# Kernel tuning notes

Measured on AMD Instinct MI355X. Metric: run time of the kernel, lower is better.

The kernel has to match this reference:

```python
import jax, jax.numpy as jnp
import numpy as np

HALF = 512   # dim // 2 == hyper_dim // 2
DIM = 1024
EPS = 1e-6


def _forward(hl, hr, xw, xh,
             qU_w, qU_b, qWu_w, qWu_b, qWb_w, qWb_b,
             kU_w, kU_b, kWu_w, kWu_b, kWb_w, kWb_b,
             alpha, beta,
             hU_w, hU_b, hWu_w, hWu_b, hWb_w, hWb_b,
             lU_w, lU_b, lWu_w, lWu_b, lWb_w, lWb_b):
    # x: (B, dim)
    x = jnp.concatenate([hl, hr], axis=1)
    # hlr: (B, 2, dim//2), xh1: (B, 1, hyper_dim//2)
    hlr = jnp.stack([hl, hr], axis=1)
    xh1 = xh[:, None, :]
    # HyperLinear: U(x) * Wu(xh) + Wb(xh); weights stored (in, out)
    q = (hlr @ qU_w + qU_b) * (xh1 @ qWu_w + qWu_b) + (xh1 @ qWb_w + qWb_b)
    k = (hlr @ kU_w + kU_b) * (xh1 @ kWu_w + kWu_b) + (xh1 @ kWb_w + kWb_b)
    # tiny 2x2 attention per sample
    scores = jax.nn.softmax(
        jnp.einsum('bqd,bkd->bqk', q, k) / jnp.sqrt(jnp.float32(HALF)), axis=-1)
    x = x + jnp.einsum('bqk,bkd->bqd', scores, hlr).reshape(x.shape[0], -1)
    # Norm: torch .std() is unbiased (ddof=1)
    mean = jnp.mean(x, axis=-1, keepdims=True)
    std = jnp.std(x, axis=-1, keepdims=True, ddof=1)
    x = alpha * (x - mean) / (std + EPS) + beta
    # hidden(x, xh) + leaf(xw, xh), both HyperLinear -> (B, dim//2)
    hidden = (x @ hU_w + hU_b) * (xh @ hWu_w + hWu_b) + (xh @ hWb_w + hWb_b)
    leaf = (xw @ lU_w + lU_b) * (xh @ lWu_w + lWu_b) + (xh @ lWb_w + lWb_b)
    return hidden + leaf


def setup_inputs() -> dict:
    key = jax.random.key(0)
    ks = jax.random.split(key, 32)
    B = 32768
    f32 = jnp.float32

    def w(k, shape, s=0.05):
        return jax.random.normal(k, shape, dtype=f32) * s

    inp = {
        'hl': jax.random.normal(ks[0], (B, HALF), dtype=f32),
        'hr': jax.random.normal(ks[1], (B, HALF), dtype=f32),
        'xw': jax.random.normal(ks[2], (B, DIM), dtype=f32),
        'xh': jax.random.normal(ks[3], (B, HALF), dtype=f32),
        # q_linear: HyperLinear(512, 512) with hyper
        'qU_w': w(ks[4], (HALF, HALF)), 'qU_b': w(ks[5], (HALF,)),
        'qWu_w': w(ks[6], (HALF, HALF)), 'qWu_b': w(ks[7], (HALF,)),
        'qWb_w': w(ks[8], (HALF, HALF)), 'qWb_b': w(ks[9], (HALF,)),
        # k_linear
        'kU_w': w(ks[10], (HALF, HALF)), 'kU_b': w(ks[11], (HALF,)),
        'kWu_w': w(ks[12], (HALF, HALF)), 'kWu_b': w(ks[13], (HALF,)),
        'kWb_w': w(ks[14], (HALF, HALF)), 'kWb_b': w(ks[15], (HALF,)),
        # Norm params over dim
        'alpha': jnp.ones((DIM,), dtype=f32),
        'beta': jnp.zeros((DIM,), dtype=f32),
        # hidden: HyperLinear(512, 1024 -> 512)
        'hU_w': w(ks[16], (DIM, HALF)), 'hU_b': w(ks[17], (HALF,)),
        'hWu_w': w(ks[18], (HALF, HALF)), 'hWu_b': w(ks[19], (HALF,)),
        'hWb_w': w(ks[20], (HALF, HALF)), 'hWb_b': w(ks[21], (HALF,)),
        # leaf: HyperLinear(512, 1024 -> 512)
        'lU_w': w(ks[22], (DIM, HALF)), 'lU_b': w(ks[23], (HALF,)),
        'lWu_w': w(ks[24], (HALF, HALF)), 'lWu_b': w(ks[25], (HALF,)),
        'lWb_w': w(ks[26], (HALF, HALF)), 'lWb_b': w(ks[27], (HALF,)),
    }
    return inp


def reference(hl, hr, xw, xh,
              qU_w, qU_b, qWu_w, qWu_b, qWb_w, qWb_b,
              kU_w, kU_b, kWu_w, kWu_b, kWb_w, kWb_b,
              alpha, beta,
              hU_w, hU_b, hWu_w, hWu_b, hWb_w, hWb_b,
              lU_w, lU_b, lWu_w, lWu_b, lWb_w, lWb_b):
    return _forward(hl, hr, xw, xh,
                    qU_w, qU_b, qWu_w, qWu_b, qWb_w, qWb_b,
                    kU_w, kU_b, kWu_w, kWu_b, kWb_w, kWb_b,
                    alpha, beta,
                    hU_w, hU_b, hWu_w, hWu_b, hWb_w, hWb_b,
                    lU_w, lU_b, lWu_w, lWu_b, lWb_w, lWb_b)
```

## Files before the change

kernel.cpp:

```cpp
#include <hip/hip_runtime.h>


typedef __attribute__((ext_vector_type(4))) float floatx4;
typedef __attribute__((ext_vector_type(8))) short shortx8;

#define NROWS 32768
#define MT 32
#define NT 64
#define BK 32
#define APAD 40
#define WMAT 262144

__device__ __forceinline__ unsigned short f2bf(float f){
  union { float f; unsigned u; } v; v.f = f;
  return (unsigned short)((v.u + 0x7fffu + ((v.u >> 16) & 1u)) >> 16);
}

struct TrArgs {
  const float* src[14];
  int off[14];
  int sc[14];
};

__global__ __launch_bounds__(256) void ktr(TrArgs ta, const float* __restrict__ alpha,
                                           unsigned short* __restrict__ wt){
  __shared__ float tile[32][33];
  const int t  = blockIdx.x >> 8;
  const int ti = blockIdx.x & 255;
  const int n0 = (ti & 15) * 32, k0 = (ti >> 4) * 32;
  const float* src = ta.src[t];
  const int off = ta.off[t], sc = ta.sc[t];
  const int r = threadIdx.x >> 5, c = threadIdx.x & 31;
#pragma unroll
  for (int p = 0; p < 4; p++){
    const int kr = p*8 + r;
    float v = src[(size_t)(off + k0 + kr)*512 + n0 + c];
    if (sc) v *= alpha[off + k0 + kr];
    tile[kr][c] = v;
  }
  __syncthreads();
#pragma unroll
  for (int p = 0; p < 4; p++){
    const int nr = p*8 + r;
    wt[(size_t)t*WMAT + (size_t)(n0+nr)*512 + k0 + c] = f2bf(tile[c][nr]);
  }
}

__global__ __launch_bounds__(256) void kst(const float* __restrict__ alpha, const float* __restrict__ beta,
                                           const float* __restrict__ hU,
                                           float* __restrict__ sp, float* __restrict__ tp){
  const int n = blockIdx.x*256 + threadIdx.x;
  float s = 0.f, t = 0.f;
  for (int k = 0; k < 1024; k++){
    const float wv = hU[(size_t)k*512 + n];
    s += alpha[k]*wv; t += beta[k]*wv;
  }
  sp[n] = s; tp[n] = t;
}

__global__ __launch_bounds__(256) void kstats(const float* __restrict__ hl, const float* __restrict__ hr,
                                              float* __restrict__ stats){
  const int w = threadIdx.x >> 6, lane = threadIdx.x & 63;
  const int row = blockIdx.x*4 + w;
  const float4* A  = (const float4*)(hl + (size_t)row*512);
  const float4* Bv = (const float4*)(hr + (size_t)row*512);
  float s1=0,s2=0,q1=0,q2=0,xc=0;
#pragma unroll
  for (int j=0;j<2;j++){
    const float4 a = A[lane + 64*j];
    const float4 b = Bv[lane + 64*j];
    s1 += a.x+a.y+a.z+a.w;
    s2 += b.x+b.y+b.z+b.w;
    q1 += a.x*a.x + a.y*a.y + a.z*a.z + a.w*a.w;
    q2 += b.x*b.x + b.y*b.y + b.z*b.z + b.w*b.w;
    xc += a.x*b.x + a.y*b.y + a.z*b.z + a.w*b.w;
  }
  for (int off=32; off; off>>=1){
    s1 += __shfl_down(s1,off); s2 += __shfl_down(s2,off);
    q1 += __shfl_down(q1,off); q2 += __shfl_down(q2,off);
    xc += __shfl_down(xc,off);
  }
  if (lane == 0){
    float* st = stats + (size_t)row*8;
    st[0]=s1; st[1]=s2; st[2]=q1; st[3]=q2; st[4]=xc;
  }
}

struct K1LDS {
  union alignas(16) {
    unsigned short stage[3*1280 + 6*2560];
    float proj[8*2112];
  } u;
  float sred[32*8*4];
};

__global__ __launch_bounds__(256,2) void k1(
    const float* __restrict__ hl, const float* __restrict__ hr, const float* __restrict__ xh,
    const unsigned short* __restrict__ wt,
    const float* __restrict__ qUb, const float* __restrict__ qWub, const float* __restrict__ qWbb,
    const float* __restrict__ kUb, const float* __restrict__ kWub, const float* __restrict__ kWbb,
    const float* __restrict__ stats, float* __restrict__ scal)
{
  __shared__ K1LDS sm;
  const int tid = threadIdx.x, w = tid >> 6, lane = tid & 63;
  const int row0 = blockIdx.x * MT;
  unsigned short* stA = sm.u.stage;
  unsigned short* stB = sm.u.stage + 3*1280;
  floatx4 acc[4][4];
  floatx4 zf; zf[0]=0.f; zf[1]=0.f; zf[2]=0.f; zf[3]=0.f;
  float s0=0.f, s1=0.f, s2=0.f, s3=0.f;
  const int erow = tid >> 3, esub = tid & 7;

  for (int dt = 0; dt < 8; dt++){
    const int d0 = dt * NT;
#pragma unroll
    for (int i=0;i<4;i++)
#pragma unroll
      for (int ns=0;ns<4;ns++) acc[i][ns] = zf;

    for (int cch = 0; cch < 16; cch++){
      const int k0 = cch * BK;
#pragma unroll
      for (int q0 = 0; q0 < 3; q0++){
        const int q = q0*256 + tid;
        const int a = q >> 8, rem = q & 255, r = rem >> 3, c4 = rem & 7;
        const float* src = (a==0) ? hl : ((a==1) ? hr : xh);
        const float4 v = *(const float4*)(src + (size_t)(row0 + r)*512 + k0 + c4*4);
        unsigned long long pk = (unsigned long long)f2bf(v.x)
                              | ((unsigned long long)f2bf(v.y) << 16)
                              | ((unsigned long long)f2bf(v.z) << 32)
                              | ((unsigned long long)f2bf(v.w) << 48);
        *(unsigned long long*)(stA + a*1280 + r*APAD + c4*4) = pk;
      }
#pragma unroll
      for (int q0 = 0; q0 < 6; q0++){
        const int q = q0*256 + tid;
        const int m = q >> 8, rem = q & 255, r = rem >> 2, c8 = rem & 3;
        *(uint4*)(stB + m*2560 + r*APAD + c8*8) =
            *(const uint4*)(wt + (size_t)m*WMAT + (size_t)(d0 + r)*512 + k0 + c8*8);
      }
      __syncthreads();
      shortx8 bfr[4];
#pragma unroll
      for (int i=0;i<4;i++){
        const int p = (w*4 + i) >> 1, ms = i & 1;
        if ((i & 1) == 0){
          const int bidx = (p < 4) ? (p >> 1) : (p - 2);
#pragma unroll
          for (int ns=0;ns<4;ns++)
            bfr[ns] = *(const shortx8*)(stB + bidx*2560 + (ns*16 + (lane & 15))*APAD + (lane >> 4)*8);
        }
        const int aidx = (p < 4) ? (p & 1) : 2;
        const shortx8 af = *(const shortx8*)(stA + aidx*1280 + (ms*16 + (lane & 15))*APAD + (lane >> 4)*8);
#pragma unroll
        for (int ns=0;ns<4;ns++)
          acc[i][ns] = __builtin_amdgcn_mfma_f32_16x16x32_bf16(af, bfr[ns], acc[i][ns], 0, 0, 0);
      }
      __syncthreads();
    }
#pragma unroll
    for (int i=0;i<4;i++){
      const int p = (w*4 + i) >> 1, ms = i & 1;
#pragma unroll
      for (int ns=0;ns<4;ns++)
#pragma unroll
        for (int r=0;r<4;r++)
          sm.u.proj[p*2112 + (ms*16 + (lane >> 4)*4 + r)*66 + ns*16 + (lane & 15)] = acc[i][ns][r];
    }
    __syncthreads();
#pragma unroll
    for (int j=0;j<8;j++){
      const int dd = esub*8 + j, gd = d0 + dd;
      const float ul = sm.u.proj[0*2112 + erow*66 + dd];
      const float ur = sm.u.proj[1*2112 + erow*66 + dd];
      const float vl = sm.u.proj[2*2112 + erow*66 + dd];
      const float vr = sm.u.proj[3*2112 + erow*66 + dd];
      const float pm = sm.u.proj[4*2112 + erow*66 + dd];
      const float pn = sm.u.proj[5*2112 + erow*66 + dd];
      const float pm2= sm.u.proj[6*2112 + erow*66 + dd];
      const float pn2= sm.u.proj[7*2112 + erow*66 + dd];
      const float f1 = pm + qWub[gd], f2 = pn + qWbb[gd];
      const float g1 = pm2 + kWub[gd], g2 = pn2 + kWbb[gd];
      const float ub = qUb[gd], kb = kUb[gd];
      const float ql = (ul + ub)*f1 + f2;
      const float qr = (ur + ub)*f1 + f2;
      const float kl = (vl + kb)*g1 + g2;
      const float kr = (vr + kb)*g1 + g2;
      s0 += ql*kl; s1 += ql*kr; s2 += qr*kl; s3 += qr*kr;
    }
    __syncthreads();
  }
  {
    float* sr = sm.sred + (erow*8 + esub)*4;
    sr[0]=s0; sr[1]=s1; sr[2]=s2; sr[3]=s3;
  }
  __syncthreads();
  if (tid < MT){
    const int row = tid;
    float t00=0,t01=0,t10=0,t11=0;
#pragma unroll
    for (int j=0;j<8;j++){
      const float* p = sm.sred + (row*8 + j)*4;
      t00+=p[0]; t01+=p[1]; t10+=p[2]; t11+=p[3];
    }
    const float isq = 0.044194173824159216f;
    t00*=isq; t01*=isq; t10*=isq; t11*=isq;
    const float m0 = fmaxf(t00,t01), m1 = fmaxf(t10,t11);
    const float e00 = expf(t00-m0), e01 = expf(t01-m0);
    const float e10 = expf(t10-m1), e11 = expf(t11-m1);
    const float p00 = e00/(e00+e01), p01 = e01/(e00+e01);
    const float p10 = e10/(e10+e11), p11 = e11/(e10+e11);
    const float* st = stats + (size_t)(row0+row)*8;
    const float S1=st[0], S2=st[1], Q1=st[2], Q2=st[3], Xc=st[4];
    const float a0=1.f+p00, a1=p01, b0=p10, b1=1.f+p11;
    const float mean = ((a0+b0)*S1 + (a1+b1)*S2) * (1.f/1024.f);
    const float ssq = (a0*a0+b0*b0)*Q1 + (a1*a1+b1*b1)*Q2 + 2.f*(a0*a1+b0*b1)*Xc;
    const float var = (ssq - 1024.f*mean*mean) * (1.f/1023.f);
    const float inv = 1.f/(sqrtf(fmaxf(var,0.f)) + 1e-6f);
    float* so = scal + (size_t)(row0+row)*8;
    so[0]=p00; so[1]=p01; so[2]=p10; so[3]=p11; so[4]=mean; so[5]=inv;
  }
}

struct K2LDS {
  union alignas(16) {
    unsigned short stage[5*1280 + 8*2560];
    float proj[9*2112];
  } u;
};

__global__ __launch_bounds__(256,2) void k2(
    const float* __restrict__ hl, const float* __restrict__ hr,
    const float* __restrict__ xh, const float* __restrict__ xw,
    const unsigned short* __restrict__ wt,
    const float* __restrict__ sp, const float* __restrict__ tp,
    const float* __restrict__ hUb, const float* __restrict__ hWub, const float* __restrict__ hWbb,
    const float* __restrict__ lUb, const float* __restrict__ lWub, const float* __restrict__ lWbb,
    const float* __restrict__ scal, float* __restrict__ out)
{
  __shared__ K2LDS sm;
  const int tid = threadIdx.x, w = tid >> 6, lane = tid & 63;
  const int row0 = blockIdx.x * MT;
  unsigned short* stA = sm.u.stage;
  unsigned short* stB = sm.u.stage + 5*1280;
  const int erow = tid >> 3, ej0 = (tid & 7)*8;
  const float* sl = scal + (size_t)(row0 + erow)*8;
  const float p00 = sl[0], p01 = sl[1], p10 = sl[2], p11 = sl[3], mean = sl[4], inv = sl[5];
  const float a0 = 1.f + p00, a1 = p01, b0 = p10, b1 = 1.f + p11;
  floatx4 acc[5][4];
  floatx4 zf; zf[0]=0.f; zf[1]=0.f; zf[2]=0.f; zf[3]=0.f;

  for (int dt = 0; dt < 8; dt++){
    const int d0 = dt * NT;
#pragma unroll
    for (int i=0;i<5;i++)
#pragma unroll
      for (int ns=0;ns<4;ns++) acc[i][ns] = zf;

    for (int cch = 0; cch < 16; cch++){
      const int k0 = cch * BK;
#pragma unroll
      for (int q0 = 0; q0 < 5; q0++){
        const int q = q0*256 + tid;
        const int a = q >> 8, rem = q & 255, r = rem >> 3, c4 = rem & 7;
        const float* srcb = (a==0) ? hl : ((a==1) ? hr : ((a==2) ? xh : xw));
        const int stride = (a >= 3) ? 1024 : 512;
        const int coff = (a == 4) ? 512 : 0;
        const float4 v = *(const float4*)(srcb + (size_t)(row0 + r)*stride + coff + k0 + c4*4);
        unsigned long long pk = (unsigned long long)f2bf(v.x)
                              | ((unsigned long long)f2bf(v.y) << 16)
                              | ((unsigned long long)f2bf(v.z) << 32)
                              | ((unsigned long long)f2bf(v.w) << 48);
        *(unsigned long long*)(stA + a*1280 + r*APAD + c4*4) = pk;
      }
#pragma unroll
      for (int q0 = 0; q0 < 8; q0++){
        const int q = q0*256 + tid;
        const int m = q >> 8, rem = q & 255, r = rem >> 2, c8 = rem & 3;
        *(uint4*)(stB + m*2560 + r*APAD + c8*8) =
            *(const uint4*)(wt + (size_t)(m+6)*WMAT + (size_t)(d0 + r)*512 + k0 + c8*8);
      }
      __syncthreads();
      shortx8 bfr[4];
      int prevB = -1;
#pragma unroll
      for (int i=0;i<5;i++){
        const int wtask = w*5 + i, p = wtask >> 1, ms = wtask & 1;
        const int bl = (p<4) ? (p>>1) : ((p<6) ? (p-2) : ((p<8) ? p : (p-4)));
        if (bl != prevB){
#pragma unroll
          for (int ns=0;ns<4;ns++)
            bfr[ns] = *(const shortx8*)(stB + bl*2560 + (ns*16 + (lane&15))*APAD + (lane>>4)*8);
          prevB = bl;
        }
        const int am = (p<4) ? (p&1) : ((p<8) ? 2 : (p-5));
        const shortx8 af = *(const shortx8*)(stA + am*1280 + (ms*16 + (lane&15))*APAD + (lane>>4)*8);
#pragma unroll
        for (int ns=0;ns<4;ns++)
          acc[i][ns] = __builtin_amdgcn_mfma_f32_16x16x32_bf16(af, bfr[ns], acc[i][ns], 0, 0, 0);
      }
      __syncthreads();
    }
#pragma unroll
    for (int i=0;i<5;i++){
      const int wtask = w*5 + i, p = wtask >> 1, ms = wtask & 1;
      const int slot = (p == 9) ? 8 : p;
#pragma unroll
      for (int ns=0;ns<4;ns++)
#pragma unroll
        for (int r=0;r<4;r++){
          float* dst = &sm.u.proj[slot*2112 + (ms*16 + (lane>>4)*4 + r)*66 + ns*16 + (lane & 15)];
          if (p == 9) *dst += acc[i][ns][r]; else *dst = acc[i][ns][r];
        }
    }
    __syncthreads();
    float res[8];
#pragma unroll
    for (int j=0;j<8;j++){
      const int dd = ej0 + j, gd = d0 + dd;
      const float A1 = sm.u.proj[0*2112 + erow*66 + dd];
      const float A2 = sm.u.proj[1*2112 + erow*66 + dd];
      const float A3 = sm.u.proj[2*2112 + erow*66 + dd];
      const float A4 = sm.u.proj[3*2112 + erow*66 + dd];
      const float Hm = sm.u.proj[4*2112 + erow*66 + dd];
      const float Hb = sm.u.proj[5*2112 + erow*66 + dd];
      const float Lm = sm.u.proj[6*2112 + erow*66 + dd];
      const float Lb = sm.u.proj[7*2112 + erow*66 + dd];
      const float Lu = sm.u.proj[8*2112 + erow*66 + dd];
      const float attnU = a0*A1 + a1*A2 + b0*A3 + b1*A4;
      const float xlnU = inv*(attnU - mean*sp[gd]) + tp[gd] + hUb[gd];
      const float hid = xlnU*(Hm + hWub[gd]) + (Hb + hWbb[gd]);
      const float lf = (Lu + lUb[gd])*(Lm + lWub[gd]) + (Lb + lWbb[gd]);
      res[j] = hid + lf;
    }
    float4 r0; r0.x=res[0]; r0.y=res[1]; r0.z=res[2]; r0.w=res[3];
    float4 r1; r1.x=res[4]; r1.y=res[5]; r1.z=res[6]; r1.w=res[7];
    float4* op = (float4*)(out + (size_t)(row0+erow)*512 + d0 + ej0);
    op[0] = r0; op[1] = r1;
    __syncthreads();
  }
}

extern "C" void kernel_launch(void* const* d_in, const int* in_sizes, int n_in,
                              void* d_out, int out_size, void* d_ws, size_t ws_size,
                              hipStream_t stream)
{
  const float* hl    = (const float*)d_in[0];
  const float* hr    = (const float*)d_in[1];
  const float* xw    = (const float*)d_in[2];
  const float* xh    = (const float*)d_in[3];
  const float* qU_w  = (const float*)d_in[4];
  const float* qU_b  = (const float*)d_in[5];
  const float* qWu_w = (const float*)d_in[6];
  const float* qWu_b = (const float*)d_in[7];
  const float* qWb_w = (const float*)d_in[8];
  const float* qWb_b = (const float*)d_in[9];
  const float* kU_w  = (const float*)d_in[10];
  const float* kU_b  = (const float*)d_in[11];
  const float* kWu_w = (const float*)d_in[12];
  const float* kWu_b = (const float*)d_in[13];
  const float* kWb_w = (const float*)d_in[14];
  const float* kWb_b = (const float*)d_in[15];
  const float* alpha = (const float*)d_in[16];
  const float* beta  = (const float*)d_in[17];
  const float* hU_w  = (const float*)d_in[18];
  const float* hU_b  = (const float*)d_in[19];
  const float* hWu_w = (const float*)d_in[20];
  const float* hWu_b = (const float*)d_in[21];
  const float* hWb_w = (const float*)d_in[22];
  const float* hWb_b = (const float*)d_in[23];
  const float* lU_w  = (const float*)d_in[24];
  const float* lU_b  = (const float*)d_in[25];
  const float* lWu_w = (const float*)d_in[26];
  const float* lWu_b = (const float*)d_in[27];
  const float* lWb_w = (const float*)d_in[28];
  const float* lWb_b = (const float*)d_in[29];

  char* ws = (char*)d_ws;
  unsigned short* wt = (unsigned short*)ws;
  float* sp    = (float*)(ws + 7340032);
  float* tp    = sp + 512;
  float* stats = (float*)(ws + 7344128);
  float* scal  = (float*)(ws + 8392704);

  TrArgs ta;
  const float* wsrc[14] = {qU_w,kU_w,qWu_w,qWb_w,kWu_w,kWb_w,hU_w,hU_w,hWu_w,hWb_w,lU_w,lU_w,lWu_w,lWb_w};
  const int woff[14] = {0,0,0,0,0,0,0,512,0,0,0,512,0,0};
  const int wsc[14]  = {0,0,0,0,0,0,1,1,0,0,0,0,0,0};
  for (int i=0;i<14;i++){ ta.src[i]=wsrc[i]; ta.off[i]=woff[i]; ta.sc[i]=wsc[i]; }

  ktr   <<<dim3(14*256),  dim3(256), 0, stream>>>(ta, alpha, wt);
  kst   <<<dim3(2),       dim3(256), 0, stream>>>(alpha, beta, hU_w, sp, tp);
  kstats<<<dim3(NROWS/4), dim3(256), 0, stream>>>(hl, hr, stats);
  k1    <<<dim3(NROWS/MT),dim3(256), 0, stream>>>(hl, hr, xh, wt,
            qU_b, qWu_b, qWb_b, kU_b, kWu_b, kWb_b, stats, scal);
  k2    <<<dim3(NROWS/MT),dim3(256), 0, stream>>>(hl, hr, xh, xw, wt, sp, tp,
            hU_b, hWu_b, hWb_b, lU_b, lWu_b, lWb_b, scal, (float*)d_out);
}
```

Measured before the change: 1.312 ms.

## Pre-convert activations to bf16, use direct global-to-LDS loads, keep epilogue in registers

Adds kernels that convert hl/hr/xh/xw to bf16 once in workspace, with the hl/hr conversion fused into the stats kernel. The GEMM kernels then stage A and B tiles with global_load_lds instead of per-tile fp32 loads and conversion. k1 is retiled to 128-wide output tiles and its epilogue computes q·k partial sums from accumulator registers with shuffle reductions rather than spilling projections to LDS. k2 likewise computes its output directly from registers. This removes the LDS round trip and the repeated conversions, at the cost of extra workspace traffic and a fallback path when the workspace is too small.

```diff
diff --git a/kernel.cpp b/kernel.cpp
--- a/kernel.cpp
+++ b/kernel.cpp
@@ -5,15 +5,24 @@
 typedef __attribute__((ext_vector_type(8))) short shortx8;
 
 #define NROWS 32768
-#define MT 32
-#define NT 64
-#define BK 32
-#define APAD 40
 #define WMAT 262144
+
+#define MFMA16(a,b,c) __builtin_amdgcn_mfma_f32_16x16x32_bf16(a,b,c,0,0,0)
 
 __device__ __forceinline__ unsigned short f2bf(float f){
   union { float f; unsigned u; } v; v.f = f;
   return (unsigned short)((v.u + 0x7fffu + ((v.u >> 16) & 1u)) >> 16);
+}
+
+__device__ __forceinline__ unsigned long long pack4(float4 v){
+  return (unsigned long long)f2bf(v.x) | ((unsigned long long)f2bf(v.y)<<16)
+       | ((unsigned long long)f2bf(v.z)<<32) | ((unsigned long long)f2bf(v.w)<<48);
+}
+
+__device__ __forceinline__ void gl_lds16(const void* g, void* l){
+  __builtin_amdgcn_global_load_lds(
+      (const __attribute__((address_space(1))) unsigned int*)g,
+      (__attribute__((address_space(3))) unsigned int*)l, 16, 0, 0);
 }
 
 struct TrArgs {
@@ -69,8 +78,7 @@
   for (int j=0;j<2;j++){
     const float4 a = A[lane + 64*j];
     const float4 b = Bv[lane + 64*j];
-    s1 += a.x+a.y+a.z+a.w;
-    s2 += b.x+b.y+b.z+b.w;
+    s1 += a.x+a.y+a.z+a.w;  s2 += b.x+b.y+b.z+b.w;
     q1 += a.x*a.x + a.y*a.y + a.z*a.z + a.w*a.w;
     q2 += b.x*b.x + b.y*b.y + b.z*b.z + b.w*b.w;
     xc += a.x*b.x + a.y*b.y + a.z*b.z + a.w*b.w;
@@ -86,122 +94,190 @@
   }
 }
 
-struct K1LDS {
-  union alignas(16) {
-    unsigned short stage[3*1280 + 6*2560];
-    float proj[8*2112];
-  } u;
-  float sred[32*8*4];
-};
-
+__global__ __launch_bounds__(256) void kconv_stats(const float* __restrict__ hl, const float* __restrict__ hr,
+                                                   unsigned short* __restrict__ hlb, unsigned short* __restrict__ hrb,
+                                                   float* __restrict__ stats){
+  const int w = threadIdx.x >> 6, lane = threadIdx.x & 63;
+  const int row = blockIdx.x*4 + w;
+  const float4* A  = (const float4*)(hl + (size_t)row*512);
+  const float4* Bv = (const float4*)(hr + (size_t)row*512);
+  float s1=0,s2=0,q1=0,q2=0,xc=0;
+#pragma unroll
+  for (int j=0;j<2;j++){
+    const float4 a = A[lane + 64*j];
+    const float4 b = Bv[lane + 64*j];
+    s1 += a.x+a.y+a.z+a.w;  s2 += b.x+b.y+b.z+b.w;
+    q1 += a.x*a.x + a.y*a.y + a.z*a.z + a.w*a.w;
+    q2 += b.x*b.x + b.y*b.y + b.z*b.z + b.w*b.w;
+    xc += a.x*b.x + a.y*b.y + a.z*b.z + a.w*b.w;
+    *(unsigned long long*)(hlb + (size_t)row*512 + (lane + 64*j)*4) = pack4(a);
+    *(unsigned long long*)(hrb + (size_t)row*512 + (lane + 64*j)*4) = pack4(b);
+  }
+  for (int off=32; off; off>>=1){
+    s1 += __shfl_down(s1,off); s2 += __shfl_down(s2,off);
+    q1 += __shfl_down(q1,off); q2 += __shfl_down(q2,off);
+    xc += __shfl_down(xc,off);
+  }
+  if (lane == 0){
+    float* st = stats + (size_t)row*8;
+    st[0]=s1; st[1]=s2; st[2]=q1; st[3]=q2; st[4]=xc;
+  }
+}
+
+__global__ __launch_bounds__(256) void kact(const float* __restrict__ xh, const float* __restrict__ xw,
+                                            unsigned short* __restrict__ xhb, unsigned short* __restrict__ xwb){
+  const int bid = blockIdx.x;
+  const float* src; unsigned short* dst; size_t base;
+  if (bid < 8192){ src = xh; dst = xhb; base = (size_t)bid*2048; }
+  else           { src = xw; dst = xwb; base = (size_t)(bid-8192)*2048; }
+  const size_t i = base + (size_t)threadIdx.x*8;
+  const float4 v0 = *(const float4*)(src + i);
+  const float4 v1 = *(const float4*)(src + i + 4);
+  unsigned long long p0 = pack4(v0), p1 = pack4(v1);
+  *(unsigned long long*)(dst + i)     = p0;
+  *(unsigned long long*)(dst + i + 4) = p1;
+}
+
+template<int PRE>
 __global__ __launch_bounds__(256,2) void k1(
     const float* __restrict__ hl, const float* __restrict__ hr, const float* __restrict__ xh,
+    const unsigned short* __restrict__ hlb, const unsigned short* __restrict__ hrb,
+    const unsigned short* __restrict__ xhb,
     const unsigned short* __restrict__ wt,
     const float* __restrict__ qUb, const float* __restrict__ qWub, const float* __restrict__ qWbb,
     const float* __restrict__ kUb, const float* __restrict__ kWub, const float* __restrict__ kWbb,
     const float* __restrict__ stats, float* __restrict__ scal)
 {
-  __shared__ K1LDS sm;
+  __shared__ __align__(16) unsigned short Ash[3*1024];
+  __shared__ __align__(16) unsigned short Bsh[6*4096];
+  __shared__ float sred[512];
   const int tid = threadIdx.x, w = tid >> 6, lane = tid & 63;
-  const int row0 = blockIdx.x * MT;
-  unsigned short* stA = sm.u.stage;
-  unsigned short* stB = sm.u.stage + 3*1280;
-  floatx4 acc[4][4];
+  const int cq = lane & 15, cr = lane >> 4;
+  const int row0 = blockIdx.x * 32;
+
+  for (int i = tid; i < 512; i += 256) sred[i] = 0.f;
+
+  floatx4 acc[8][2][2];
   floatx4 zf; zf[0]=0.f; zf[1]=0.f; zf[2]=0.f; zf[3]=0.f;
-  float s0=0.f, s1=0.f, s2=0.f, s3=0.f;
-  const int erow = tid >> 3, esub = tid & 7;
-
-  for (int dt = 0; dt < 8; dt++){
-    const int d0 = dt * NT;
-#pragma unroll
-    for (int i=0;i<4;i++)
-#pragma unroll
-      for (int ns=0;ns<4;ns++) acc[i][ns] = zf;
-
-    for (int cch = 0; cch < 16; cch++){
-      const int k0 = cch * BK;
-#pragma unroll
-      for (int q0 = 0; q0 < 3; q0++){
-        const int q = q0*256 + tid;
-        const int a = q >> 8, rem = q & 255, r = rem >> 3, c4 = rem & 7;
-        const float* src = (a==0) ? hl : ((a==1) ? hr : xh);
-        const float4 v = *(const float4*)(src + (size_t)(row0 + r)*512 + k0 + c4*4);
-        unsigned long long pk = (unsigned long long)f2bf(v.x)
-                              | ((unsigned long long)f2bf(v.y) << 16)
-                              | ((unsigned long long)f2bf(v.z) << 32)
-                              | ((unsigned long long)f2bf(v.w) << 48);
-        *(unsigned long long*)(stA + a*1280 + r*APAD + c4*4) = pk;
-      }
-#pragma unroll
-      for (int q0 = 0; q0 < 6; q0++){
-        const int q = q0*256 + tid;
-        const int m = q >> 8, rem = q & 255, r = rem >> 2, c8 = rem & 3;
-        *(uint4*)(stB + m*2560 + r*APAD + c8*8) =
-            *(const uint4*)(wt + (size_t)m*WMAT + (size_t)(d0 + r)*512 + k0 + c8*8);
+
+#pragma unroll 1
+  for (int dt = 0; dt < 4; dt++){
+    const int d0 = dt * 128;
+#pragma unroll
+    for (int p=0;p<8;p++)
+#pragma unroll
+      for (int ms=0;ms<2;ms++){ acc[p][ms][0]=zf; acc[p][ms][1]=zf; }
+
+#pragma unroll 1
+    for (int cc = 0; cc < 16; cc++){
+      const int k0 = cc * 32;
+      if (PRE){
+#pragma unroll
+        for (int j=0;j<2;j++){
+          const int idx = j*256 + tid;
+          if (idx < 384){
+            const int a = idx>>7, wi = idx&127, r = wi>>2, kg = wi&3;
+            const unsigned short* s = (a==0) ? hlb : ((a==1) ? hrb : xhb);
+            gl_lds16(s + (size_t)(row0+r)*512 + k0 + kg*8, Ash + idx*8);
+          }
+        }
+      } else {
+#pragma unroll
+        for (int a=0;a<3;a++){
+          const int r = tid>>3, c4 = tid&7;
+          const float* s = (a==0) ? hl : ((a==1) ? hr : xh);
+          const float4 v = *(const float4*)(s + (size_t)(row0+r)*512 + k0 + c4*4);
+          *(unsigned long long*)(Ash + a*1024 + r*32 + c4*4) = pack4(v);
+        }
+      }
+#pragma unroll
+      for (int j=0;j<12;j++){
+        const int idx = j*256 + tid;
+        const int m = idx>>9, wi = idx&511, r = wi>>2, kg = wi&3;
+        gl_lds16(wt + (size_t)m*WMAT + (size_t)(d0+r)*512 + k0 + kg*8, Bsh + idx*8);
       }
       __syncthreads();
-      shortx8 bfr[4];
-#pragma unroll
-      for (int i=0;i<4;i++){
-        const int p = (w*4 + i) >> 1, ms = i & 1;
-        if ((i & 1) == 0){
-          const int bidx = (p < 4) ? (p >> 1) : (p - 2);
-#pragma unroll
-          for (int ns=0;ns<4;ns++)
-            bfr[ns] = *(const shortx8*)(stB + bidx*2560 + (ns*16 + (lane & 15))*APAD + (lane >> 4)*8);
-        }
-        const int aidx = (p < 4) ? (p & 1) : 2;
-        const shortx8 af = *(const shortx8*)(stA + aidx*1280 + (ms*16 + (lane & 15))*APAD + (lane >> 4)*8);
-#pragma unroll
-        for (int ns=0;ns<4;ns++)
-          acc[i][ns] = __builtin_amdgcn_mfma_f32_16x16x32_bf16(af, bfr[ns], acc[i][ns], 0, 0, 0);
+      shortx8 af[3][2], bf[6];
+#pragma unroll
+      for (int a=0;a<3;a++)
+#pragma unroll
+        for (int ms=0;ms<2;ms++)
+          af[a][ms] = *(const shortx8*)(Ash + a*1024 + (ms*16+cq)*32 + cr*8);
+#pragma unroll
+      for (int n=0;n<2;n++){
+#pragma unroll
+        for (int m=0;m<6;m++)
+          bf[m] = *(const shortx8*)(Bsh + m*4096 + (w*32 + n*16 + cq)*32 + cr*8);
+#pragma unroll
+        for (int ms=0;ms<2;ms++){
+          acc[0][ms][n] = MFMA16(af[0][ms], bf[0], acc[0][ms][n]);
+          acc[1][ms][n] = MFMA16(af[1][ms], bf[0], acc[1][ms][n]);
+          acc[2][ms][n] = MFMA16(af[0][ms], bf[1], acc[2][ms][n]);
+          acc[3][ms][n] = MFMA16(af[1][ms], bf[1], acc[3][ms][n]);
+          acc[4][ms][n] = MFMA16(af[2][ms], bf[2], acc[4][ms][n]);
+          acc[5][ms][n] = MFMA16(af[2][ms], bf[3], acc[5][ms][n]);
+          acc[6][ms][n] = MFMA16(af[2][ms], bf[4], acc[6][ms][n]);
+          acc[7][ms][n] = MFMA16(af[2][ms], bf[5], acc[7][ms][n]);
+        }
       }
       __syncthreads();
     }
-#pragma unroll
-    for (int i=0;i<4;i++){
-      const int p = (w*4 + i) >> 1, ms = i & 1;
-#pragma unroll
-      for (int ns=0;ns<4;ns++)
+    float qub[2], qwu[2], qwb[2], kub[2], kwu[2], kwb[2];
+#pragma unroll
+    for (int n=0;n<2;n++){
+      const int col = d0 + w*32 + n*16 + cq;
+      qub[n]=qUb[col]; qwu[n]=qWub[col]; qwb[n]=qWbb[col];
+      kub[n]=kUb[col]; kwu[n]=kWub[col]; kwb[n]=kWbb[col];
+    }
+    float sc[2][4][4];
+#pragma unroll
+    for (int ms=0;ms<2;ms++)
+#pragma unroll
+      for (int r=0;r<4;r++){ sc[ms][r][0]=0.f; sc[ms][r][1]=0.f; sc[ms][r][2]=0.f; sc[ms][r][3]=0.f; }
+#pragma unroll
+    for (int ms=0;ms<2;ms++)
+#pragma unroll
+      for (int n=0;n<2;n++)
+#pragma unroll
+        for (int r=0;r<4;r++){
+          const float ul = acc[0][ms][n][r], ur = acc[1][ms][n][r];
+          const float vl = acc[2][ms][n][r], vr = acc[3][ms][n][r];
+          const float f1 = acc[4][ms][n][r] + qwu[n], f2 = acc[5][ms][n][r] + qwb[n];
+          const float g1 = acc[6][ms][n][r] + kwu[n], g2 = acc[7][ms][n][r] + kwb[n];
+          const float ql = (ul + qub[n])*f1 + f2, qr = (ur + qub[n])*f1 + f2;
+          const float kl = (vl + kub[n])*g1 + g2, kr = (vr + kub[n])*g1 + g2;
+          sc[ms][r][0] += ql*kl; sc[ms][r][1] += ql*kr;
+          sc[ms][r][2] += qr*kl; sc[ms][r][3] += qr*kr;
+        }
+#pragma unroll
+    for (int b=1;b<16;b<<=1)
+#pragma unroll
+      for (int ms=0;ms<2;ms++)
 #pragma unroll
         for (int r=0;r<4;r++)
-          sm.u.proj[p*2112 + (ms*16 + (lane >> 4)*4 + r)*66 + ns*16 + (lane & 15)] = acc[i][ns][r];
+#pragma unroll
+          for (int c=0;c<4;c++)
+            sc[ms][r][c] += __shfl_xor(sc[ms][r][c], b);
+    if (cq == 0){
+#pragma unroll
+      for (int ms=0;ms<2;ms++)
+#pragma unroll
+        for (int r=0;r<4;r++){
+          const int row = ms*16 + cr*4 + r;
+#pragma unroll
+          for (int c=0;c<4;c++)
+            sred[w*128 + row*4 + c] += sc[ms][r][c];
+        }
     }
-    __syncthreads();
-#pragma unroll
-    for (int j=0;j<8;j++){
-      const int dd = esub*8 + j, gd = d0 + dd;
-      const float ul = sm.u.proj[0*2112 + erow*66 + dd];
-      const float ur = sm.u.proj[1*2112 + erow*66 + dd];
-      const float vl = sm.u.proj[2*2112 + erow*66 + dd];
-      const float vr = sm.u.proj[3*2112 + erow*66 + dd];
-      const float pm = sm.u.proj[4*2112 + erow*66 + dd];
-      const float pn = sm.u.proj[5*2112 + erow*66 + dd];
-      const float pm2= sm.u.proj[6*2112 + erow*66 + dd];
-      const float pn2= sm.u.proj[7*2112 + erow*66 + dd];
-      const float f1 = pm + qWub[gd], f2 = pn + qWbb[gd];
-      const float g1 = pm2 + kWub[gd], g2 = pn2 + kWbb[gd];
-      const float ub = qUb[gd], kb = kUb[gd];
-      const float ql = (ul + ub)*f1 + f2;
-      const float qr = (ur + ub)*f1 + f2;
-      const float kl = (vl + kb)*g1 + g2;
-      const float kr = (vr + kb)*g1 + g2;
-      s0 += ql*kl; s1 += ql*kr; s2 += qr*kl; s3 += qr*kr;
-    }
-    __syncthreads();
-  }
-  {
-    float* sr = sm.sred + (erow*8 + esub)*4;
-    sr[0]=s0; sr[1]=s1; sr[2]=s2; sr[3]=s3;
   }
   __syncthreads();
-  if (tid < MT){
+  if (tid < 32){
     const int row = tid;
     float t00=0,t01=0,t10=0,t11=0;
 #pragma unroll
-    for (int j=0;j<8;j++){
-      const float* p = sm.sred + (row*8 + j)*4;
-      t00+=p[0]; t01+=p[1]; t10+=p[2]; t11+=p[3];
+    for (int w2=0;w2<4;w2++){
+      const int base = w2*128 + row*4;
+      t00+=sred[base+0]; t01+=sred[base+1]; t10+=sred[base+2]; t11+=sred[base+3];
     }
     const float isq = 0.044194173824159216f;
     t00*=isq; t01*=isq; t10*=isq; t11*=isq;
@@ -222,122 +298,117 @@
   }
 }
 
-struct K2LDS {
-  union alignas(16) {
-    unsigned short stage[5*1280 + 8*2560];
-    float proj[9*2112];
-  } u;
-};
-
+template<int PRE>
 __global__ __launch_bounds__(256,2) void k2(
     const float* __restrict__ hl, const float* __restrict__ hr,
     const float* __restrict__ xh, const float* __restrict__ xw,
+    const unsigned short* __restrict__ hlb, const unsigned short* __restrict__ hrb,
+    const unsigned short* __restrict__ xhb, const unsigned short* __restrict__ xwb,
     const unsigned short* __restrict__ wt,
     const float* __restrict__ sp, const float* __restrict__ tp,
     const float* __restrict__ hUb, const float* __restrict__ hWub, const float* __restrict__ hWbb,
     const float* __restrict__ lUb, const float* __restrict__ lWub, const float* __restrict__ lWbb,
     const float* __restrict__ scal, float* __restrict__ out)
 {
-  __shared__ K2LDS sm;
+  __shared__ __align__(16) unsigned short Ash[5*1024];
+  __shared__ __align__(16) unsigned short Bsh[8*2048];
+  __shared__ float scs[256];
   const int tid = threadIdx.x, w = tid >> 6, lane = tid & 63;
-  const int row0 = blockIdx.x * MT;
-  unsigned short* stA = sm.u.stage;
-  unsigned short* stB = sm.u.stage + 5*1280;
-  const int erow = tid >> 3, ej0 = (tid & 7)*8;
-  const float* sl = scal + (size_t)(row0 + erow)*8;
-  const float p00 = sl[0], p01 = sl[1], p10 = sl[2], p11 = sl[3], mean = sl[4], inv = sl[5];
-  const float a0 = 1.f + p00, a1 = p01, b0 = p10, b1 = 1.f + p11;
-  floatx4 acc[5][4];
+  const int cq = lane & 15, cr = lane >> 4;
+  const int row0 = blockIdx.x * 32;
+
+  scs[tid] = scal[(size_t)row0*8 + tid];
+
+  floatx4 acc[10][2];
   floatx4 zf; zf[0]=0.f; zf[1]=0.f; zf[2]=0.f; zf[3]=0.f;
 
+#pragma unroll 1
   for (int dt = 0; dt < 8; dt++){
-    const int d0 = dt * NT;
-#pragma unroll
-    for (int i=0;i<5;i++)
-#pragma unroll
-      for (int ns=0;ns<4;ns++) acc[i][ns] = zf;
-
-    for (int cch = 0; cch < 16; cch++){
-      const int k0 = cch * BK;
-#pragma unroll
-      for (int q0 = 0; q0 < 5; q0++){
-        const int q = q0*256 + tid;
-        const int a = q >> 8, rem = q & 255, r = rem >> 3, c4 = rem & 7;
-        const float* srcb = (a==0) ? hl : ((a==1) ? hr : ((a==2) ? xh : xw));
-        const int stride = (a >= 3) ? 1024 : 512;
-        const int coff = (a == 4) ? 512 : 0;
-        const float4 v = *(const float4*)(srcb + (size_t)(row0 + r)*stride + coff + k0 + c4*4);
-        unsigned long long pk = (unsigned long long)f2bf(v.x)
-                              | ((unsigned long long)f2bf(v.y) << 16)
-                              | ((unsigned long long)f2bf(v.z) << 32)
-                              | ((unsigned long long)f2bf(v.w) << 48);
-        *(unsigned long long*)(stA + a*1280 + r*APAD + c4*4) = pk;
-      }
-#pragma unroll
-      for (int q0 = 0; q0 < 8; q0++){
-        const int q = q0*256 + tid;
-        const int m = q >> 8, rem = q & 255, r = rem >> 2, c8 = rem & 3;
-        *(uint4*)(stB + m*2560 + r*APAD + c8*8) =
-            *(const uint4*)(wt + (size_t)(m+6)*WMAT + (size_t)(d0 + r)*512 + k0 + c8*8);
+    const int d0 = dt * 64;
+#pragma unroll
+    for (int p=0;p<10;p++){ acc[p][0]=zf; acc[p][1]=zf; }
+
+#pragma unroll 1
+    for (int cc = 0; cc < 16; cc++){
+      const int k0 = cc * 32;
+      if (PRE){
+#pragma unroll
+        for (int j=0;j<3;j++){
+          const int idx = j*256 + tid;
+          if (idx < 640){
+            const int a = idx>>7, wi = idx&127, r = wi>>2, kg = wi&3;
+            const unsigned short* s;
+            size_t off;
+            if (a < 3){ s = (a==0) ? hlb : ((a==1) ? hrb : xhb);
+                        off = (size_t)(row0+r)*512 + k0 + kg*8; }
+            else      { s = xwb;
+                        off = (size_t)(row0+r)*1024 + (a==4 ? 512 : 0) + k0 + kg*8; }
+            gl_lds16(s + off, Ash + idx*8);
+          }
+        }
+      } else {
+#pragma unroll
+        for (int a=0;a<5;a++){
+          const int r = tid>>3, c4 = tid&7;
+          const float* s = (a==0) ? hl : ((a==1) ? hr : ((a==2) ? xh : xw));
+          const int stride = (a>=3) ? 1024 : 512;
+          const int coff = (a==4) ? 512 : 0;
+          const float4 v = *(const float4*)(s + (size_t)(row0+r)*stride + coff + k0 + c4*4);
+          *(unsigned long long*)(Ash + a*1024 + r*32 + c4*4) = pack4(v);
+        }
+      }
+#pragma unroll
+      for (int j=0;j<8;j++){
+        const int idx = j*256 + tid;
+        const int m = idx>>8, wi = idx&255, r = wi>>2, kg = wi&3;
+        gl_lds16(wt + (size_t)(6+m)*WMAT + (size_t)(d0+r)*512 + k0 + kg*8, Bsh + idx*8);
       }
       __syncthreads();
-      shortx8 bfr[4];
-      int prevB = -1;
-#pragma unroll
-      for (int i=0;i<5;i++){
-        const int wtask = w*5 + i, p = wtask >> 1, ms = wtask & 1;
-        const int bl = (p<4) ? (p>>1) : ((p<6) ? (p-2) : ((p<8) ? p : (p-4)));
-        if (bl != prevB){
-#pragma unroll
-          for (int ns=0;ns<4;ns++)
-            bfr[ns] = *(const shortx8*)(stB + bl*2560 + (ns*16 + (lane&15))*APAD + (lane>>4)*8);
-          prevB = bl;
-        }
-        const int am = (p<4) ? (p&1) : ((p<8) ? 2 : (p-5));
-        const shortx8 af = *(const shortx8*)(stA + am*1280 + (ms*16 + (lane&15))*APAD + (lane>>4)*8);
-#pragma unroll
-        for (int ns=0;ns<4;ns++)
-          acc[i][ns] = __builtin_amdgcn_mfma_f32_16x16x32_bf16(af, bfr[ns], acc[i][ns], 0, 0, 0);
+      shortx8 af[5][2], bf[8];
+#pragma unroll
+      for (int a=0;a<5;a++)
+#pragma unroll
+        for (int ms=0;ms<2;ms++)
+          af[a][ms] = *(const shortx8*)(Ash + a*1024 + (ms*16+cq)*32 + cr*8);
+#pragma unroll
+      for (int m=0;m<8;m++)
+        bf[m] = *(const shortx8*)(Bsh + m*2048 + (w*16 + cq)*32 + cr*8);
+#pragma unroll
+      for (int ms=0;ms<2;ms++){
+        acc[0][ms] = MFMA16(af[0][ms], bf[0], acc[0][ms]);
+        acc[1][ms] = MFMA16(af[1][ms], bf[0], acc[1][ms]);
+        acc[2][ms] = MFMA16(af[0][ms], bf[1], acc[2][ms]);
+        acc[3][ms] = MFMA16(af[1][ms], bf[1], acc[3][ms]);
+        acc[4][ms] = MFMA16(af[2][ms], bf[2], acc[4][ms]);
+        acc[5][ms] = MFMA16(af[2][ms], bf[3], acc[5][ms]);
+        acc[6][ms] = MFMA16(af[2][ms], bf[6], acc[6][ms]);
+        acc[7][ms] = MFMA16(af[2][ms], bf[7], acc[7][ms]);
+        acc[8][ms] = MFMA16(af[3][ms], bf[4], acc[8][ms]);
+        acc[9][ms] = MFMA16(af[4][ms], bf[5], acc[9][ms]);
       }
       __syncthreads();
     }
-#pragma unroll
-    for (int i=0;i<5;i++){
-      const int wtask = w*5 + i, p = wtask >> 1, ms = wtask & 1;
-      const int slot = (p == 9) ? 8 : p;
-#pragma unroll
-      for (int ns=0;ns<4;ns++)
-#pragma unroll
-        for (int r=0;r<4;r++){
-          float* dst = &sm.u.proj[slot*2112 + (ms*16 + (lane>>4)*4 + r)*66 + ns*16 + (lane & 15)];
-          if (p == 9) *dst += acc[i][ns][r]; else *dst = acc[i][ns][r];
-        }
-    }
-    __syncthreads();
-    float res[8];
-#pragma unroll
-    for (int j=0;j<8;j++){
-      const int dd = ej0 + j, gd = d0 + dd;
-      const float A1 = sm.u.proj[0*2112 + erow*66 + dd];
-      const float A2 = sm.u.proj[1*2112 + erow*66 + dd];
-      const float A3 = sm.u.proj[2*2112 + erow*66 + dd];
-      const float A4 = sm.u.proj[3*2112 + erow*66 + dd];
-      const float Hm = sm.u.proj[4*2112 + erow*66 + dd];
-      const float Hb = sm.u.proj[5*2112 + erow*66 + dd];
-      const float Lm = sm.u.proj[6*2112 + erow*66 + dd];
-      const float Lb = sm.u.proj[7*2112 + erow*66 + dd];
-      const float Lu = sm.u.proj[8*2112 + erow*66 + dd];
-      const float attnU = a0*A1 + a1*A2 + b0*A3 + b1*A4;
-      const float xlnU = inv*(attnU - mean*sp[gd]) + tp[gd] + hUb[gd];
-      const float hid = xlnU*(Hm + hWub[gd]) + (Hb + hWbb[gd]);
-      const float lf = (Lu + lUb[gd])*(Lm + lWub[gd]) + (Lb + lWbb[gd]);
-      res[j] = hid + lf;
-    }
-    float4 r0; r0.x=res[0]; r0.y=res[1]; r0.z=res[2]; r0.w=res[3];
-    float4 r1; r1.x=res[4]; r1.y=res[5]; r1.z=res[6]; r1.w=res[7];
-    float4* op = (float4*)(out + (size_t)(row0+erow)*512 + d0 + ej0);
-    op[0] = r0; op[1] = r1;
-    __syncthreads();
+    const int col = d0 + w*16 + cq;
+    const float spv = sp[col],  tpv = tp[col],  hub = hUb[col];
+    const float hwub = hWub[col], hwbb = hWbb[col];
+    const float lub = lUb[col], lwub = lWub[col], lwbb = lWbb[col];
+#pragma unroll
+    for (int ms=0;ms<2;ms++)
+#pragma unroll
+      for (int r=0;r<4;r++){
+        const int row = ms*16 + cr*4 + r;
+        const float p00 = scs[row*8+0], p01 = scs[row*8+1];
+        const float p10 = scs[row*8+2], p11 = scs[row*8+3];
+        const float mean = scs[row*8+4], inv = scs[row*8+5];
+        const float a0 = 1.f+p00, a1 = p01, b0 = p10, b1 = 1.f+p11;
+        const float attnU = a0*acc[0][ms][r] + a1*acc[1][ms][r]
+                          + b0*acc[2][ms][r] + b1*acc[3][ms][r];
+        const float xlnU = inv*(attnU - mean*spv) + tpv + hub;
+        const float hid = xlnU*(acc[4][ms][r] + hwub) + (acc[5][ms][r] + hwbb);
+        const float lf  = (acc[8][ms][r] + acc[9][ms][r] + lub)*(acc[6][ms][r] + lwub)
+                        + (acc[7][ms][r] + lwbb);
+        out[(size_t)(row0+row)*512 + col] = hid + lf;
+      }
   }
 }
 
@@ -382,6 +453,12 @@
   float* tp    = sp + 512;
   float* stats = (float*)(ws + 7344128);
   float* scal  = (float*)(ws + 8392704);
+  unsigned short* hlb = (unsigned short*)(ws + 9441280);
+  unsigned short* hrb = hlb + 16777216;
+  unsigned short* xhb = hrb + 16777216;
+  unsigned short* xwb = xhb + 16777216;
+  const size_t NEED = 9441280ull + 3ull*33554432ull + 67108864ull;
+  const bool pre = (ws_size >= NEED);
 
   TrArgs ta;
   const float* wsrc[14] = {qU_w,kU_w,qWu_w,qWb_w,kWu_w,kWb_w,hU_w,hU_w,hWu_w,hWb_w,lU_w,lU_w,lWu_w,lWb_w};
@@ -389,11 +466,21 @@
   const int wsc[14]  = {0,0,0,0,0,0,1,1,0,0,0,0,0,0};
   for (int i=0;i<14;i++){ ta.src[i]=wsrc[i]; ta.off[i]=woff[i]; ta.sc[i]=wsc[i]; }
 
-  ktr   <<<dim3(14*256),  dim3(256), 0, stream>>>(ta, alpha, wt);
-  kst   <<<dim3(2),       dim3(256), 0, stream>>>(alpha, beta, hU_w, sp, tp);
-  kstats<<<dim3(NROWS/4), dim3(256), 0, stream>>>(hl, hr, stats);
-  k1    <<<dim3(NROWS/MT),dim3(256), 0, stream>>>(hl, hr, xh, wt,
-            qU_b, qWu_b, qWb_b, kU_b, kWu_b, kWb_b, stats, scal);
-  k2    <<<dim3(NROWS/MT),dim3(256), 0, stream>>>(hl, hr, xh, xw, wt, sp, tp,
-            hU_b, hWu_b, hWb_b, lU_b, lWu_b, lWb_b, scal, (float*)d_out);
-}
+  ktr<<<dim3(14*256), dim3(256), 0, stream>>>(ta, alpha, wt);
+  kst<<<dim3(2),      dim3(256), 0, stream>>>(alpha, beta, hU_w, sp, tp);
+
+  if (pre){
+    kconv_stats<<<dim3(NROWS/4), dim3(256), 0, stream>>>(hl, hr, hlb, hrb, stats);
+    kact<<<dim3(24576), dim3(256), 0, stream>>>(xh, xw, xhb, xwb);
+    k1<1><<<dim3(NROWS/32), dim3(256), 0, stream>>>(hl, hr, xh, hlb, hrb, xhb, wt,
+        qU_b, qWu_b, qWb_b, kU_b, kWu_b, kWb_b, stats, scal);
+    k2<1><<<dim3(NROWS/32), dim3(256), 0, stream>>>(hl, hr, xh, xw, hlb, hrb, xhb, xwb, wt,
+        sp, tp, hU_b, hWu_b, hWb_b, lU_b, lWu_b, lWb_b, scal, (float*)d_out);
+  } else {
+    kstats<<<dim3(NROWS/4), dim3(256), 0, stream>>>(hl, hr, stats);
+    k1<0><<<dim3(NROWS/32), dim3(256), 0, stream>>>(hl, hr, xh, hlb, hrb, xhb, wt,
+        qU_b, qWu_b, qWb_b, kU_b, kWu_b, kWb_b, stats, scal);
+    k2<0><<<dim3(NROWS/32), dim3(256), 0, stream>>>(hl, hr, xh, xw, hlb, hrb, xhb, xwb, wt,
+        sp, tp, hU_b, hWu_b, hWb_b, lU_b, lWu_b, lWb_b, scal, (float*)d_out);
+  }
+}
```

After: 1.144 ms. 1.15x faster.
